# Kernel tuning notes

Hardware: AMD Instinct MI355X
Metric: run time of the kernel (lower is better)

## Reference

```python
import jax, jax.numpy as jnp
import numpy as np

B, C, P, NP = 16, 768, 2048, 64
FFE = 4


def _ln(x, g, b, eps=1e-5):
    m = jnp.mean(x, axis=-1, keepdims=True)
    v = jnp.mean(jnp.square(x - m), axis=-1, keepdims=True)
    return (x - m) * jax.lax.rsqrt(v + eps) * g + b


def _gelu(x):
    return jax.nn.gelu(x, approximate=False)  # torch nn.GELU default (erf)


def _any_attn(q, k, v, nqg, nqb, nkg, nkb, nvg, nvb, wq, wk, wv, wp, bq, bk, bv, bp):
    # AnyAttention: LN each stream, project, ReLU-gated logits scaled by d^-0.5, softmax, proj
    scale = q.shape[-1] ** -0.5
    qn = _ln(q, nqg, nqb) @ wq + bq
    kn = _ln(k, nkg, nkb) @ wk + bk
    vn = _ln(v, nvg, nvb) @ wv + bv
    attn = jnp.einsum('bqc,bkc->bqk', qn, kn)
    attn = jax.nn.relu(attn) * scale  # returned attn is relu*scale (pre-softmax)
    out = jnp.einsum('bqk,bkc->bqc', jax.nn.softmax(attn, axis=-1), vn)
    return attn, out @ wp + bp


def _forward(x, parts,
             enc_nq_g, enc_nq_b, enc_nk_g, enc_nk_b, enc_nv_g, enc_nv_b,
             enc_wq, enc_wk, enc_wv, enc_wp, enc_bq, enc_bk, enc_bv, enc_bp,
             dec_nq_g, dec_nq_b, dec_nk_g, dec_nk_b, dec_nv_g, dec_nv_b,
             dec_wq, dec_wk, dec_wv, dec_wp, dec_bq, dec_bk, dec_bv, dec_bp,
             ffn_ng, ffn_nb, ffn_w1, ffn_b1, ffn_w2, ffn_b2,
             sr_w1, sr_b1, sr_w2, sr_b2):
    x = jnp.swapaxes(x, 1, 2)  # b c p -> b p c
    # SimpleReasoning: SE-style gate over part tokens (AdaptiveMaxPool1d(1) = max over channel dim)
    g = jnp.max(parts, axis=-1)                                  # [b, np]
    g = _gelu(g @ sr_w1 + sr_b1)
    gate = jax.nn.sigmoid(g @ sr_w2 + sr_b2)[..., None]          # [b, np, 1]
    parts = gate * parts + parts                                 # parts1 + parts (residual)
    # enc_attn: parts attend over image tokens
    attn0, attn_out = _any_attn(parts, x, x,
                                enc_nq_g, enc_nq_b, enc_nk_g, enc_nk_b, enc_nv_g, enc_nv_b,
                                enc_wq, enc_wk, enc_wv, enc_wp, enc_bq, enc_bk, enc_bv, enc_bp)
    attn_0 = jnp.max(attn0, axis=-1)                             # maxpool over k -> [b, np]
    parts_in = parts + attn_out
    # FFN on image tokens with residual
    h = _ln(x, ffn_ng, ffn_nb)
    feats1 = x + (_gelu(h @ ffn_w1 + ffn_b1) @ ffn_w2 + ffn_b2)
    # dec_attn: image tokens attend over part tokens
    _, feats = _any_attn(feats1, parts_in, parts_in,
                         dec_nq_g, dec_nq_b, dec_nk_g, dec_nk_b, dec_nv_g, dec_nv_b,
                         dec_wq, dec_wk, dec_wv, dec_wp, dec_bq, dec_bk, dec_bv, dec_bp)
    feats = x + feats
    return jnp.swapaxes(feats, 1, 2), attn_0                     # [b, c, p], [b, np]


def setup_inputs() -> dict:
    key = jax.random.key(0)
    ki = iter(jax.random.split(key, 48))
    def rn(shape, s=1.0):
        return jax.random.normal(next(ki), shape, jnp.float32) * s
    d = {}
    d['x'] = rn((B, C, P))
    d['parts'] = rn((B, NP, C))
    for pre in ('enc', 'dec'):
        for nm in ('nq', 'nk', 'nv'):
            d[f'{pre}_{nm}_g'] = jnp.ones((C,), jnp.float32)
            d[f'{pre}_{nm}_b'] = jnp.zeros((C,), jnp.float32)
        for nm in ('wq', 'wk', 'wv', 'wp'):
            d[f'{pre}_{nm}'] = rn((C, C), 0.02)
        for nm in ('bq', 'bk', 'bv', 'bp'):
            d[f'{pre}_{nm}'] = jnp.zeros((C,), jnp.float32)
    d['ffn_ng'] = jnp.ones((C,), jnp.float32)
    d['ffn_nb'] = jnp.zeros((C,), jnp.float32)
    d['ffn_w1'] = rn((C, FFE * C), 0.02)
    d['ffn_b1'] = jnp.zeros((FFE * C,), jnp.float32)
    d['ffn_w2'] = rn((FFE * C, C), 0.02)
    d['ffn_b2'] = jnp.zeros((C,), jnp.float32)
    d['sr_w1'] = rn((NP, NP), 0.1)
    d['sr_b1'] = jnp.zeros((NP,), jnp.float32)
    d['sr_w2'] = rn((NP, NP), 0.1)
    d['sr_b2'] = jnp.zeros((NP,), jnp.float32)
    return d


def reference(x, parts,
              enc_nq_g, enc_nq_b, enc_nk_g, enc_nk_b, enc_nv_g, enc_nv_b,
              enc_wq, enc_wk, enc_wv, enc_wp, enc_bq, enc_bk, enc_bv, enc_bp,
              dec_nq_g, dec_nq_b, dec_nk_g, dec_nk_b, dec_nv_g, dec_nv_b,
              dec_wq, dec_wk, dec_wv, dec_wp, dec_bq, dec_bk, dec_bv, dec_bp,
              ffn_ng, ffn_nb, ffn_w1, ffn_b1, ffn_w2, ffn_b2,
              sr_w1, sr_b1, sr_w2, sr_b2):
    return _forward(x, parts,
                    enc_nq_g, enc_nq_b, enc_nk_g, enc_nk_b, enc_nv_g, enc_nv_b,
                    enc_wq, enc_wk, enc_wv, enc_wp, enc_bq, enc_bk, enc_bv, enc_bp,
                    dec_nq_g, dec_nq_b, dec_nk_g, dec_nk_b, dec_nv_g, dec_nv_b,
                    dec_wq, dec_wk, dec_wv, dec_wp, dec_bq, dec_bk, dec_bv, dec_bp,
                    ffn_ng, ffn_nb, ffn_w1, ffn_b1, ffn_w2, ffn_b2,
                    sr_w1, sr_b1, sr_w2, sr_b2)
```

## Files before the change

kernel.cpp:

```cpp
#include <hip/hip_runtime.h>

typedef unsigned short u16;
typedef unsigned int u32;
typedef __bf16 bf16x8 __attribute__((ext_vector_type(8)));
typedef float f32x4 __attribute__((ext_vector_type(4)));
typedef unsigned int u32x4 __attribute__((ext_vector_type(4)));

#define BB 16
#define CC 768
#define PP 2048
#define FF 3072

__device__ __forceinline__ float b2f(u16 u) {
  unsigned int x = ((unsigned int)u) << 16;
  return __builtin_bit_cast(float, x);
}
__device__ __forceinline__ u16 f2b(float f) {
  unsigned int x = __builtin_bit_cast(unsigned int, f);
  x += 0x7fffu + ((x >> 16) & 1u);
  return (u16)(x >> 16);
}
__device__ __forceinline__ float erf_fast(float x) {
  float ax = fabsf(x);
  float t = 1.0f / fmaf(0.3275911f, ax, 1.0f);
  float p = t * fmaf(t, fmaf(t, fmaf(t, fmaf(t, 1.061405429f, -1.453152027f),
                                     1.421413741f), -0.284496736f), 0.254829592f);
  float r = 1.0f - p * __expf(-ax * ax);
  return copysignf(r, x);
}
__device__ __forceinline__ float gelu_f(float x) {
  return 0.5f * x * (1.0f + erf_fast(x * 0.7071067811865475f));
}

typedef __attribute__((address_space(1))) const unsigned int g_u32;
typedef __attribute__((address_space(3))) unsigned int l_u32;
__device__ __forceinline__ void gl_lds16(const u16* g, u16* l) {
  __builtin_amdgcn_global_load_lds((g_u32*)g, (l_u32*)l, 16, 0, 0);
}

struct Wtr10 {
  const float* W[10]; const float* g[10]; u16* O[10]; int Kd[10]; int Nd[10];
};
__global__ void wtr10_k(Wtr10 a) {
  __shared__ float t[64][65];
  int tbid = blockIdx.x;
  int z, bx, by;
  if (tbid < 1152) { z = tbid / 144; int r = tbid % 144; bx = r % 12; by = r / 12; }
  else if (tbid < 1728) { z = 8; int r = tbid - 1152; bx = r % 48; by = r / 48; }
  else { z = 9; int r = tbid - 1728; bx = r % 12; by = r / 12; }
  const float* W = a.W[z];
  const float* g = a.g[z];
  u16* Wt = a.O[z];
  int K = a.Kd[z], N = a.Nd[z];
  int n0 = bx * 64, k0 = by * 64;
  int tx = threadIdx.x & 63, ty = threadIdx.x >> 6;
  for (int i = 0; i < 16; ++i) {
    int k = k0 + ty + i * 4;
    float sc = g ? g[k] : 1.0f;
    t[ty + i * 4][tx] = W[(long)k * N + n0 + tx] * sc;
  }
  __syncthreads();
  for (int i = 0; i < 16; ++i) {
    int n = n0 + ty + i * 4;
    Wt[(long)n * K + k0 + tx] = f2b(t[tx][ty + i * 4]);
  }
}

struct Bf7 {
  const float* b[7]; const float* nb[7]; const float* W[7]; float* o[7];
  int Kd[7]; int Nd[7];
};
__global__ void bfuse7_k(Bf7 a) {
  __shared__ float red[4][64];
  int tbid = blockIdx.x;
  int z, bx;
  if (tbid < 72) { z = tbid / 12; bx = tbid % 12; }
  else { z = 6; bx = tbid - 72; }
  const float* b = a.b[z];
  const float* nb = a.nb[z];
  const float* W = a.W[z];
  float* outb = a.o[z];
  int K = a.Kd[z], N = a.Nd[z];
  int n = bx * 64 + (threadIdx.x & 63);
  int slice = threadIdx.x >> 6;
  float acc = 0.f;
#pragma unroll 4
  for (int k = slice; k < K; k += 4) acc += nb[k] * W[(long)k * N + n];
  red[slice][threadIdx.x & 63] = acc;
  __syncthreads();
  if (slice == 0)
    outb[n] = b[n] + red[0][threadIdx.x & 63] + red[1][threadIdx.x & 63] +
              red[2][threadIdx.x & 63] + red[3][threadIdx.x & 63];
}

__global__ void xprep_k(const float* __restrict__ x, float* __restrict__ mean,
                        float* __restrict__ rstd, u16* __restrict__ xh) {
  __shared__ float t[64][65];
  __shared__ float red[8][64];
  __shared__ float mn_s[64], rs_s[64];
  int p0 = blockIdx.x * 64, b = blockIdx.y;
  int tx = threadIdx.x & 63, ty = threadIdx.x >> 6;
  const float* xb = x + (long)b * CC * PP;
  float s = 0.f, sq = 0.f;
  for (int c = ty; c < CC; c += 4) {
    float f = xb[(long)c * PP + p0 + tx];
    s += f; sq += f * f;
  }
  red[ty][tx] = s;
  red[4 + ty][tx] = sq;
  __syncthreads();
  if (ty == 0) {
    float S = red[0][tx] + red[1][tx] + red[2][tx] + red[3][tx];
    float Q = red[4][tx] + red[5][tx] + red[6][tx] + red[7][tx];
    float m = S * (1.0f / 768.0f);
    float var = Q * (1.0f / 768.0f) - m * m;
    float rs = rsqrtf(var + 1e-5f);
    mn_s[tx] = m; rs_s[tx] = rs;
    int gi = (b << 11) + p0 + tx;
    mean[gi] = m; rstd[gi] = rs;
  }
  __syncthreads();
  u16* ob = xh + (long)b * PP * CC;
  for (int cb = 0; cb < 12; ++cb) {
    int c0 = cb * 64;
    for (int i = 0; i < 16; ++i)
      t[ty + i * 4][tx] = xb[(long)(c0 + ty + i * 4) * PP + p0 + tx];
    __syncthreads();
    for (int i = 0; i < 16; ++i) {
      int pl = ty + i * 4;
      ob[(long)(p0 + pl) * CC + c0 + tx] = f2b((t[tx][pl] - mn_s[pl]) * rs_s[pl]);
    }
    __syncthreads();
  }
}

__global__ void parts_gate_k(const float* __restrict__ parts,
                             const float* __restrict__ w1, const float* __restrict__ b1,
                             const float* __restrict__ w2, const float* __restrict__ b2,
                             float* __restrict__ gate_out) {
  int b = blockIdx.x, t = threadIdx.x;
  __shared__ float g[64], g1[64];
  int r = t >> 2, l4 = t & 3;
  const float* pr = parts + ((long)b * 64 + r) * CC;
  float m = -1e30f;
  for (int c = l4; c < CC; c += 4) m = fmaxf(m, pr[c]);
  m = fmaxf(m, __shfl_xor(m, 1));
  m = fmaxf(m, __shfl_xor(m, 2));
  if (l4 == 0) g[r] = m;
  __syncthreads();
  if (t < 64) {
    float a = b1[t];
    for (int k = 0; k < 64; ++k) a += g[k] * w1[k * 64 + t];
    g1[t] = gelu_f(a);
  }
  __syncthreads();
  if (t < 64) {
    float a = b2[t];
    for (int k = 0; k < 64; ++k) a += g1[k] * w2[k * 64 + t];
    gate_out[b * 64 + t] = 1.0f / (1.0f + expf(-a));
  }
}

__global__ void gate_ln_k(const float* __restrict__ parts, const float* __restrict__ gate,
                          float* __restrict__ parts1, u16* __restrict__ ph) {
  int row = blockIdx.x * 4 + (threadIdx.x >> 6);
  int lane = threadIdx.x & 63;
  float g = 1.0f + gate[row];
  const float* ip = parts + (long)row * CC;
  float* op1 = parts1 + (long)row * CC;
  float v[12];
  float s = 0.f, sq = 0.f;
  for (int i = 0; i < 12; ++i) {
    float f = ip[lane + i * 64] * g;
    v[i] = f; op1[lane + i * 64] = f;
    s += f; sq += f * f;
  }
  for (int o = 32; o; o >>= 1) { s += __shfl_xor(s, o); sq += __shfl_xor(sq, o); }
  float mean = s * (1.0f / 768.0f);
  float var = sq * (1.0f / 768.0f) - mean * mean;
  float rstd = rsqrtf(var + 1e-5f);
  u16* op = ph + (long)row * CC;
  for (int i = 0; i < 12; ++i) op[lane + i * 64] = f2b((v[i] - mean) * rstd);
}

template <typename T>
__global__ void ln_rows_k(const T* __restrict__ in, u16* __restrict__ outp, int rows) {
  int row = blockIdx.x * 4 + (threadIdx.x >> 6);
  if (row >= rows) return;
  int lane = threadIdx.x & 63;
  const T* ip = in + (long)row * CC;
  float v[12];
  float s = 0.f, sq = 0.f;
  for (int i = 0; i < 12; ++i) {
    float f;
    if constexpr (sizeof(T) == 2) f = b2f(((const u16*)ip)[lane + i * 64]);
    else f = ((const float*)ip)[lane + i * 64];
    v[i] = f; s += f; sq += f * f;
  }
  for (int o = 32; o; o >>= 1) { s += __shfl_xor(s, o); sq += __shfl_xor(sq, o); }
  float mean = s * (1.0f / 768.0f);
  float var = sq * (1.0f / 768.0f) - mean * mean;
  float rstd = rsqrtf(var + 1e-5f);
  u16* op = outp + (long)row * CC;
  for (int i = 0; i < 12; ++i) op[lane + i * 64] = f2b((v[i] - mean) * rstd);
}

__global__ void softmax_enc_k(const float* __restrict__ attn, u16* __restrict__ sm,
                              float* __restrict__ attn0) {
  int row = blockIdx.x * 4 + (threadIdx.x >> 6);
  int lane = threadIdx.x & 63;
  const float* ap = attn + (long)row * PP;
  float v[32];
  float m = -1e30f;
  for (int i = 0; i < 32; ++i) { v[i] = ap[lane + i * 64]; m = fmaxf(m, v[i]); }
  for (int o = 32; o; o >>= 1) m = fmaxf(m, __shfl_xor(m, o));
  float s = 0.f;
  for (int i = 0; i < 32; ++i) { float e = expf(v[i] - m); v[i] = e; s += e; }
  for (int o = 32; o; o >>= 1) s += __shfl_xor(s, o);
  float inv = 1.0f / s;
  u16* sp = sm + (long)row * PP;
  for (int i = 0; i < 32; ++i) sp[lane + i * 64] = f2b(v[i] * inv);
  if (lane == 0) attn0[row] = m;
}

__global__ void pvred_k(const float* __restrict__ part, u16* __restrict__ outp) {
  long i = (long)blockIdx.x * 256 + threadIdx.x;
  const f32x4* p = (const f32x4*)part;
  f32x4 a = p[i];
  a += p[i + 196608];
  a += p[i + 2 * 196608];
  a += p[i + 3 * 196608];
  u32 lo = (u32)f2b(a.x) | ((u32)f2b(a.y) << 16);
  u32 hi = (u32)f2b(a.z) | ((u32)f2b(a.w) << 16);
  ((u32*)outp)[i * 2] = lo;
  ((u32*)outp)[i * 2 + 1] = hi;
}

template <int EPI>
__global__ __launch_bounds__(256) void gemmf_k(
    const u16* __restrict__ A, const u16* __restrict__ Bm, void* __restrict__ Cm,
    const float* __restrict__ bias, int M, int N, int K,
    const u16* __restrict__ rxh, const float* __restrict__ rmean,
    const float* __restrict__ rrstd, long rro, const float* __restrict__ res32) {
  __shared__ __align__(16) u16 As[128 * 32];
  __shared__ __align__(16) u16 Bs[128 * 32];
  const int nbx = N >> 7;
  const int nwg = gridDim.x;
  int tile = blockIdx.x;
  if ((nwg & 7) == 0) {
    tile = (tile & 7) * (nwg >> 3) + (tile >> 3);
  }
  const int bm0 = (tile / nbx) << 7;
  const int bn0 = (tile % nbx) << 7;
  const int tid = threadIdx.x;
  const int lane = tid & 63;
  const int wave = tid >> 6;
  const int laneq = lane & 15, lanek = lane >> 4;
  const int wm = (wave >> 1) << 6, wn = (wave & 1) << 6;
  const int srow = wave * 32 + (lane >> 2);
  const int scol = (lane & 3) << 3;
  const u16* Ag0 = A + (long)(bm0 + srow) * K + scol;
  const u16* Ag1 = A + (long)(bm0 + srow + 16) * K + scol;
  const u16* Bg0 = Bm + (long)(bn0 + srow) * K + scol;
  const u16* Bg1 = Bm + (long)(bn0 + srow + 16) * K + scol;
  u16* lA0 = As + wave * 1024;
  u16* lA1 = As + wave * 1024 + 512;
  u16* lB0 = Bs + wave * 1024;
  u16* lB1 = Bs + wave * 1024 + 512;
  f32x4 acc[4][4] = {};
  for (int k0 = 0; k0 < K; k0 += 32) {
    gl_lds16(Ag0 + k0, lA0);
    gl_lds16(Ag1 + k0, lA1);
    gl_lds16(Bg0 + k0, lB0);
    gl_lds16(Bg1 + k0, lB1);
    __syncthreads();
    bf16x8 af[4], bfr[4];
#pragma unroll
    for (int i = 0; i < 4; ++i)
      af[i] = *(const bf16x8*)(As + (wm + i * 16 + laneq) * 32 + (lanek << 3));
#pragma unroll
    for (int i = 0; i < 4; ++i)
      bfr[i] = *(const bf16x8*)(Bs + (wn + i * 16 + laneq) * 32 + (lanek << 3));
#pragma unroll
    for (int mi = 0; mi < 4; ++mi)
#pragma unroll
      for (int ni = 0; ni < 4; ++ni)
        acc[mi][ni] =
            __builtin_amdgcn_mfma_f32_16x16x32_bf16(af[mi], bfr[ni], acc[mi][ni], 0, 0, 0);
    __syncthreads();
  }
#pragma unroll
  for (int mi = 0; mi < 4; ++mi) {
#pragma unroll
    for (int r = 0; r < 4; ++r) {
      const int row = bm0 + wm + mi * 16 + (lanek << 2) + r;
      float mn = 0.f, istd = 0.f;
      if constexpr (EPI == 3) {
        long gr = rro + row;
        mn = rmean[gr];
        istd = 1.0f / rrstd[gr];
      }
#pragma unroll
      for (int ni = 0; ni < 4; ++ni) {
        const int col = bn0 + wn + ni * 16 + laneq;
        float v = acc[mi][ni][r] + bias[col];
        long off = (long)row * N + col;
        if constexpr (EPI == 0) {
          ((u16*)Cm)[off] = f2b(v);
        } else if constexpr (EPI == 1) {
          ((u16*)Cm)[off] = f2b(gelu_f(v));
        } else if constexpr (EPI == 3) {
          v += b2f(rxh[(rro + row) * 768 + col]) * istd + mn;
          ((u16*)Cm)[off] = f2b(v);
        } else {
          ((float*)Cm)[off] = v + res32[off];
        }
      }
    }
  }
}

#define G256_BAR() __builtin_amdgcn_s_barrier()
#define G256_WLGKM0()                                    \
  do {                                                   \
    asm volatile("s_waitcnt lgkmcnt(0)" ::: "memory");   \
    __builtin_amdgcn_sched_barrier(0);                   \
  } while (0)
#define G256_RD_A(HALF)                                                        \
  _Pragma("unroll") for (int m2 = 0; m2 < 4; ++m2) {                           \
    af[m2 * 2 + 0] = *(const bf16x8*)(Ab + ar + (HALF)*4096 + m2 * 1024 + g0); \
    af[m2 * 2 + 1] = *(const bf16x8*)(Ab + ar + (HALF)*4096 + m2 * 1024 + g1); \
  }
#define G256_RD_B(HALF, BFR)                                                   \
  _Pragma("unroll") for (int n2 = 0; n2 < 2; ++n2) {                           \
    BFR[n2 * 2 + 0] = *(const bf16x8*)(Bb + br + (HALF)*2048 + n2 * 1024 + g0);\
    BFR[n2 * 2 + 1] = *(const bf16x8*)(Bb + br + (HALF)*2048 + n2 * 1024 + g1);\
  }
#define G256_MFMA_Q(H, NH, BFR)                                                \
  __builtin_amdgcn_s_setprio(1);                                               \
  _Pragma("unroll") for (int m2 = 0; m2 < 4; ++m2)                             \
  _Pragma("unroll") for (int n2 = 0; n2 < 2; ++n2)                             \
  _Pragma("unroll") for (int s = 0; s < 2; ++s)                                \
      acc[(H)*4 + m2][(NH)*2 + n2] = __builtin_amdgcn_mfma_f32_16x16x32_bf16(  \
          af[m2 * 2 + s], BFR[n2 * 2 + s], acc[(H)*4 + m2][(NH)*2 + n2], 0, 0, 0); \
  __builtin_amdgcn_s_setprio(0);

template <int EPI>
__global__ __launch_bounds__(512, 2) void gemm256_k(
    const u16* __restrict__ A, const u16* __restrict__ Bm, void* __restrict__ Cm,
    const float* __restrict__ bias, int M, int N, int K,
    const u16* __restrict__ rxh, const float* __restrict__ rmean,
    const float* __restrict__ rrstd, long rro) {
  __shared__ __align__(16) u16 As[2 * 16384];
  __shared__ __align__(16) u16 Bs[2 * 16384];
  const int nbx = N >> 8;
  const int nwg = gridDim.x;
  int tile = blockIdx.x;
  if ((nwg & 7) == 0) {
    tile = (tile & 7) * (nwg >> 3) + (tile >> 3);
  }
  const int bm0 = (tile / nbx) << 8;
  const int bn0 = (tile % nbx) << 8;
  const int tid = threadIdx.x;
  const int lane = tid & 63;
  const int wave = tid >> 6;
  const int laneq = lane & 15, lanek = lane >> 4;
  const int wrow = (wave >> 2) << 7;
  const int wcol = (wave & 3) << 6;
  const int srow8 = lane >> 3;
  const int sg = (lane & 7) ^ srow8;
  const u16* gA = A + (long)(bm0 + wave * 8 + srow8) * K + sg * 8;
  const u16* gB = Bm + (long)(bn0 + wave * 8 + srow8) * K + sg * 8;
  const long lineK = (long)64 * K;
  const int ldsLine = wave * 512;
  const int gx = laneq & 7;
  const int g0 = ((lanek) ^ gx) << 3;
  const int g1 = ((lanek + 4) ^ gx) << 3;
  const int ar = (wrow + laneq) * 64;
  const int br = (wcol + laneq) * 64;
  f32x4 acc[8][4] = {};
  bf16x8 af[8], bfr0[4], bfr1[4];
  const int NT = K >> 6;

  {
    u16* dA = (u16*)As;
    u16* dB = (u16*)Bs;
    gl_lds16(gA, dA + ldsLine);
    gl_lds16(gA + lineK, dA + ldsLine + 4096);
    gl_lds16(gA + 2 * lineK, dA + ldsLine + 8192);
    gl_lds16(gA + 3 * lineK, dA + ldsLine + 12288);
    gl_lds16(gB, dB + ldsLine);
    gl_lds16(gB + lineK, dB + ldsLine + 4096);
    gl_lds16(gB + 2 * lineK, dB + ldsLine + 8192);
    gl_lds16(gB + 3 * lineK, dB + ldsLine + 12288);
  }
  for (int T = 0; T < NT; ++T) {
    const u16* Ab = As + (T & 1) * 16384;
    const u16* Bb = Bs + (T & 1) * 16384;
    u16* An = (u16*)As + ((T & 1) ^ 1) * 16384;
    u16* Bn = (u16*)Bs + ((T & 1) ^ 1) * 16384;
    const long ko = (long)(T + 1) * 64;
    const bool more = (T + 1 < NT);
    if (more) {
      gl_lds16(gA + ko, An + ldsLine);
      gl_lds16(gA + ko + lineK, An + ldsLine + 4096);
      gl_lds16(gB + ko, Bn + ldsLine);
      gl_lds16(gB + ko + lineK, Bn + ldsLine + 4096);
      asm volatile("s_waitcnt vmcnt(4)" ::: "memory");
    } else {
      asm volatile("s_waitcnt vmcnt(0)" ::: "memory");
    }
    G256_BAR();
    G256_RD_A(0);
    G256_RD_B(0, bfr0);
    G256_WLGKM0();
    G256_MFMA_Q(0, 0, bfr0);
    G256_BAR();
    if (more) {
      gl_lds16(gA + ko + 2 * lineK, An + ldsLine + 8192);
      gl_lds16(gA + ko + 3 * lineK, An + ldsLine + 12288);
      gl_lds16(gB + ko + 2 * lineK, Bn + ldsLine + 8192);
      gl_lds16(gB + ko + 3 * lineK, Bn + ldsLine + 12288);
    }
    G256_RD_B(1, bfr1);
    G256_BAR();
    G256_WLGKM0();
    G256_MFMA_Q(0, 1, bfr1);
    G256_BAR();
    G256_RD_A(1);
    G256_BAR();
    G256_WLGKM0();
    G256_MFMA_Q(1, 1, bfr1);
    G256_BAR();
    G256_MFMA_Q(1, 0, bfr0);
  }

#pragma unroll
  for (int mi = 0; mi < 8; ++mi) {
#pragma unroll
    for (int r = 0; r < 4; ++r) {
      const int row = bm0 + wrow + mi * 16 + (lanek << 2) + r;
      float mn = 0.f, istd = 0.f;
      if constexpr (EPI == 3) {
        long gr = rro + row;
        mn = rmean[gr];
        istd = 1.0f / rrstd[gr];
      }
#pragma unroll
      for (int ni = 0; ni < 4; ++ni) {
        const int col = bn0 + wcol + ni * 16 + laneq;
        float v = acc[mi][ni][r] + bias[col];
        long off = (long)row * N + col;
        if constexpr (EPI == 0) {
          ((u16*)Cm)[off] = f2b(v);
        } else if constexpr (EPI == 1) {
          ((u16*)Cm)[off] = f2b(gelu_f(v));
        } else {
          v += b2f(rxh[(rro + row) * 768 + col]) * istd + mn;
          ((u16*)Cm)[off] = f2b(v);
        }
      }
    }
  }
}

template <int EPI, bool BNT, int TM, int TN>
__global__ __launch_bounds__(256) void gemm_k(
    const u16* __restrict__ A, const u16* __restrict__ Bm, void* __restrict__ Cm,
    const float* __restrict__ bias, int M, int N, int kLen, int lda, int ldB,
    long sA, long sB, long sC, float scale, const float* __restrict__ res32) {
  __shared__ __align__(16) u16 As[TM][40];
  __shared__ __align__(16) u16 Bs[TN][40];
  const int bn0 = blockIdx.x * TN;
  const int bm0 = (EPI == 4) ? 0 : blockIdx.y * TM;
  const int kOff = (EPI == 4) ? blockIdx.y * kLen : 0;
  const int bz = blockIdx.z;
  const u16* Ab = A + (long)bz * sA;
  const u16* Bb = Bm + (long)bz * sB;
  const long coff = (EPI == 4) ? ((long)blockIdx.y * gridDim.z + bz) * sC
                               : (long)bz * sC;
  const int tid = threadIdx.x;
  const int lane = tid & 63;
  const int wave = tid >> 6;
  const int wm = (TM == 64) ? 0 : ((TN == 64) ? wave * 32 : ((wave >> 1) << 6));
  const int wn = (TN == 64) ? 0 : ((TM == 64) ? wave * 32 : ((wave & 1) << 6));
  constexpr int MI = (TN == 64) ? 2 : 4;
  constexpr int NI = (TM == 64) ? 2 : 4;
  const int laneq = lane & 15, lanek = lane >> 4;
  f32x4 acc[MI][NI] = {};
  for (int k0 = 0; k0 < kLen; k0 += 32) {
    __syncthreads();
#pragma unroll
    for (int j = 0; j < TM / 64; ++j) {
      int v = tid + j * 256;
      int m = v >> 2, kcl = (v & 3) << 3;
      u32x4 val = {0, 0, 0, 0};
      if (bm0 + m < M)
        val = *(const u32x4*)(Ab + (long)(bm0 + m) * lda + kOff + k0 + kcl);
      *(u32x4*)(&As[m][kcl]) = val;
    }
    if constexpr (BNT) {
#pragma unroll
      for (int j = 0; j < TN / 64; ++j) {
        int v = tid + j * 256;
        int n = v >> 2, kcl = (v & 3) << 3;
        u32x4 val = {0, 0, 0, 0};
        if (bn0 + n < N)
          val = *(const u32x4*)(Bb + (long)(bn0 + n) * ldB + kOff + k0 + kcl);
        *(u32x4*)(&Bs[n][kcl]) = val;
      }
    } else {
      constexpr int CCH = TN / 8;
#pragma unroll
      for (int j = 0; j < TN / 64; ++j) {
        int v = tid + j * 256;
        int kk = v / CCH, nc = (v % CCH) << 3;
        u32x4 val = {0, 0, 0, 0};
        if (bn0 + nc < N)
          val = *(const u32x4*)(Bb + (long)(kOff + k0 + kk) * ldB + bn0 + nc);
        union { u32x4 v4; u16 u[8]; } uu;
        uu.v4 = val;
#pragma unroll
        for (int e = 0; e < 8; ++e) Bs[nc + e][kk] = uu.u[e];
      }
    }
    __syncthreads();
    bf16x8 af[MI], bfr[NI];
#pragma unroll
    for (int i = 0; i < MI; ++i)
      af[i] = *(const bf16x8*)(&As[wm + i * 16 + laneq][lanek << 3]);
#pragma unroll
    for (int i = 0; i < NI; ++i)
      bfr[i] = *(const bf16x8*)(&Bs[wn + i * 16 + laneq][lanek << 3]);
#pragma unroll
    for (int mi = 0; mi < MI; ++mi)
#pragma unroll
      for (int ni = 0; ni < NI; ++ni)
        acc[mi][ni] =
            __builtin_amdgcn_mfma_f32_16x16x32_bf16(af[mi], bfr[ni], acc[mi][ni], 0, 0, 0);
  }
  if constexpr (EPI == 5) {
    __syncthreads();
    float* smem = (float*)(wave < 2 ? (void*)As : (void*)Bs) + (wave & 1) * 1024;
    const int pbase = bm0 + wm + (lane & 3) * 16;
    const long obase = (long)bz * CC * PP;
#pragma unroll
    for (int ni = 0; ni < 4; ++ni) {
#pragma unroll
      for (int mi = 0; mi < 4; ++mi)
#pragma unroll
        for (int r = 0; r < 4; ++r) {
          const int col = bn0 + wn + ni * 16 + laneq;
          smem[(mi * 16 + (lanek << 2) + r) * 16 + laneq] = acc[mi][ni][r] + bias[col];
        }
      const int c = bn0 + wn + ni * 16 + (lane >> 2);
      const float* xs = res32 + obase + (long)c * PP + pbase;
      float* os = (float*)Cm + obase + (long)c * PP + pbase;
      const float* sr = smem + (lane & 3) * 256 + (lane >> 2);
#pragma unroll
      for (int q4 = 0; q4 < 4; ++q4) {
        f32x4 xv = *(const f32x4*)(xs + q4 * 4);
        f32x4 ov;
        ov.x = sr[(q4 * 4 + 0) * 16] + xv.x;
        ov.y = sr[(q4 * 4 + 1) * 16] + xv.y;
        ov.z = sr[(q4 * 4 + 2) * 16] + xv.z;
        ov.w = sr[(q4 * 4 + 3) * 16] + xv.w;
        *(f32x4*)(os + q4 * 4) = ov;
      }
    }
  } else if constexpr (EPI == 6) {
#pragma unroll
    for (int mi = 0; mi < MI; ++mi) {
#pragma unroll
      for (int r = 0; r < 4; ++r) {
        float e[NI];
        float mx = -1e30f;
#pragma unroll
        for (int ni = 0; ni < NI; ++ni) {
          float v = fmaxf(acc[mi][ni][r], 0.0f) * scale;
          e[ni] = v;
          mx = fmaxf(mx, v);
        }
        mx = fmaxf(mx, __shfl_xor(mx, 1));
        mx = fmaxf(mx, __shfl_xor(mx, 2));
        mx = fmaxf(mx, __shfl_xor(mx, 4));
        mx = fmaxf(mx, __shfl_xor(mx, 8));
        float s = 0.f;
#pragma unroll
        for (int ni = 0; ni < NI; ++ni) { e[ni] = __expf(e[ni] - mx); s += e[ni]; }
        s += __shfl_xor(s, 1);
        s += __shfl_xor(s, 2);
        s += __shfl_xor(s, 4);
        s += __shfl_xor(s, 8);
        float inv = 1.0f / s;
        const int row = bm0 + wm + mi * 16 + (lanek << 2) + r;
#pragma unroll
        for (int ni = 0; ni < NI; ++ni) {
          const int col = bn0 + wn + ni * 16 + laneq;
          ((u16*)Cm)[coff + (long)row * N + col] = f2b(e[ni] * inv);
        }
      }
    }
  } else {
#pragma unroll
    for (int mi = 0; mi < MI; ++mi) {
#pragma unroll
      for (int ni = 0; ni < NI; ++ni) {
        int col = bn0 + wn + ni * 16 + laneq;
        if (col >= N) continue;
#pragma unroll
        for (int r = 0; r < 4; ++r) {
          int row = bm0 + wm + mi * 16 + (lanek << 2) + r;
          if (row >= M) continue;
          float v = acc[mi][ni][r];
          long off = coff + (long)row * N + col;
          if constexpr (EPI == 0) {
            if (bias) v += bias[col];
            ((u16*)Cm)[off] = f2b(v);
          } else if constexpr (EPI == 2) {
            ((float*)Cm)[off] = fmaxf(v, 0.0f) * scale;
          } else {
            ((float*)Cm)[off] = v;
          }
        }
      }
    }
  }
}

extern "C" void kernel_launch(void* const* d_in, const int* in_sizes, int n_in,
                              void* d_out, int out_size, void* d_ws, size_t ws_size,
                              hipStream_t stream) {
  (void)in_sizes; (void)n_in; (void)out_size;
  const float* x        = (const float*)d_in[0];
  const float* parts    = (const float*)d_in[1];
  const float* enc_nq_g = (const float*)d_in[2];
  const float* enc_nq_b = (const float*)d_in[3];
  const float* enc_nk_g = (const float*)d_in[4];
  const float* enc_nk_b = (const float*)d_in[5];
  const float* enc_nv_g = (const float*)d_in[6];
  const float* enc_nv_b = (const float*)d_in[7];
  const float* enc_wq   = (const float*)d_in[8];
  const float* enc_wk   = (const float*)d_in[9];
  const float* enc_wv   = (const float*)d_in[10];
  const float* enc_wp   = (const float*)d_in[11];
  const float* enc_bq   = (const float*)d_in[12];
  const float* enc_bk   = (const float*)d_in[13];
  const float* enc_bv   = (const float*)d_in[14];
  const float* enc_bp   = (const float*)d_in[15];
  const float* dec_nq_g = (const float*)d_in[16];
  const float* dec_nq_b = (const float*)d_in[17];
  const float* dec_nk_g = (const float*)d_in[18];
  const float* dec_nk_b = (const float*)d_in[19];
  const float* dec_nv_g = (const float*)d_in[20];
  const float* dec_nv_b = (const float*)d_in[21];
  const float* dec_wq   = (const float*)d_in[22];
  const float* dec_wk   = (const float*)d_in[23];
  const float* dec_wv   = (const float*)d_in[24];
  const float* dec_wp   = (const float*)d_in[25];
  const float* dec_bq   = (const float*)d_in[26];
  const float* dec_bk   = (const float*)d_in[27];
  const float* dec_bv   = (const float*)d_in[28];
  const float* dec_bp   = (const float*)d_in[29];
  const float* ffn_ng   = (const float*)d_in[30];
  const float* ffn_nb   = (const float*)d_in[31];
  const float* ffn_w1   = (const float*)d_in[32];
  const float* ffn_b1   = (const float*)d_in[33];
  const float* ffn_w2   = (const float*)d_in[34];
  const float* ffn_b2   = (const float*)d_in[35];
  const float* sr_w1    = (const float*)d_in[36];
  const float* sr_b1    = (const float*)d_in[37];
  const float* sr_w2    = (const float*)d_in[38];
  const float* sr_b2    = (const float*)d_in[39];
  float* outp = (float*)d_out;

  char* base = (char*)d_ws;
  size_t used = 0;
  auto alloc = [&](size_t bytes) -> void* {
    void* p = base + used;
    used += (bytes + 255) & ~(size_t)255;
    return p;
  };
  const long MC = (long)CC * CC;
  u16* WqeT  = (u16*)alloc(MC * 2);
  u16* WkvT  = (u16*)alloc(MC * 2 * 2);
  u16* WpeT  = (u16*)alloc(MC * 2);
  u16* WqdT  = (u16*)alloc(MC * 2);
  u16* WkvdT = (u16*)alloc(MC * 2 * 2);
  u16* WpdT  = (u16*)alloc(MC * 2);
  u16* W1T   = (u16*)alloc((long)CC * FF * 2);
  u16* W2T   = (u16*)alloc((long)CC * FF * 2);
  float* bqe  = (float*)alloc(CC * 4);
  float* bkv  = (float*)alloc(2 * CC * 4);
  float* bqd  = (float*)alloc(CC * 4);
  float* bkvd = (float*)alloc(2 * CC * 4);
  float* b1f  = (float*)alloc(FF * 4);
  float* meanx = (float*)alloc((long)BB * PP * 4);
  float* rstdx = (float*)alloc((long)BB * PP * 4);
  const long BPC = (long)BB * PP * CC;
  u16* bufA = (u16*)alloc(BPC * 2);
  u16* bufB = (u16*)alloc(BPC * 2);
  u16* bufC = (u16*)alloc(BPC * 2);
  u16* kv = bufB;
  const long PC = (long)BB * 64 * CC;
  float* parts1   = (float*)alloc(PC * 4);
  float* gateb    = (float*)alloc((long)BB * 64 * 4);
  u16*   p1hat    = (u16*)alloc(PC * 2);
  u16*   qn_e     = (u16*)alloc(PC * 2);
  float* attn_e   = (float*)alloc((long)BB * 64 * PP * 4);
  u16*   sm_e     = (u16*)alloc((long)BB * 64 * PP * 2);
  u16*   pv_e     = (u16*)alloc(PC * 2);
  float* pvpart   = (float*)alloc((long)4 * PC * 4);
  float* parts_in = (float*)alloc(PC * 4);
  u16*   pin_hat  = (u16*)alloc(PC * 2);
  u16*   kvd      = (u16*)alloc(PC * 2 * 2);
  u16*   vwT      = (u16*)alloc(PC * 2);
  u16*   sm_d     = (u16*)alloc((long)BB * PP * 64 * 2);
  int chunk_rows = 16384;
  while (chunk_rows > 4096 &&
         used + (size_t)chunk_rows * FF * 2 > ws_size)
    chunk_rows >>= 1;
  u16* ff1 = (u16*)alloc((long)chunk_rows * FF * 2);
  if (used > ws_size) return;

  const float scale = 0.03608439182435161f;
  dim3 blk(256);
  dim3 blk2(512);

  {
    Wtr10 wa;
    const float* Ws[10] = {enc_wq, enc_wk, enc_wv, enc_wp, dec_wq, dec_wk,
                           dec_wv, dec_wp, ffn_w1, ffn_w2};
    const float* gs[10] = {enc_nq_g, enc_nk_g, enc_nv_g, nullptr, dec_nq_g,
                           dec_nk_g, dec_nv_g, nullptr, ffn_ng, nullptr};
    u16* Os[10] = {WqeT, WkvT, WkvT + MC, WpeT, WqdT, WkvdT, WkvdT + MC, WpdT,
                   W1T, W2T};
    int Ks[10] = {CC, CC, CC, CC, CC, CC, CC, CC, CC, FF};
    int Ns[10] = {CC, CC, CC, CC, CC, CC, CC, CC, FF, CC};
    for (int i = 0; i < 10; ++i) {
      wa.W[i] = Ws[i]; wa.g[i] = gs[i]; wa.O[i] = Os[i];
      wa.Kd[i] = Ks[i]; wa.Nd[i] = Ns[i];
    }
    wtr10_k<<<2304, blk, 0, stream>>>(wa);
    Bf7 ba;
    const float* bs[7] = {enc_bq, enc_bk, enc_bv, dec_bq, dec_bk, dec_bv, ffn_b1};
    const float* nbs[7] = {enc_nq_b, enc_nk_b, enc_nv_b, dec_nq_b, dec_nk_b,
                           dec_nv_b, ffn_nb};
    const float* ws[7] = {enc_wq, enc_wk, enc_wv, dec_wq, dec_wk, dec_wv, ffn_w1};
    float* os[7] = {bqe, bkv, bkv + CC, bqd, bkvd, bkvd + CC, b1f};
    int Ks2[7] = {CC, CC, CC, CC, CC, CC, CC};
    int Ns2[7] = {CC, CC, CC, CC, CC, CC, FF};
    for (int i = 0; i < 7; ++i) {
      ba.b[i] = bs[i]; ba.nb[i] = nbs[i]; ba.W[i] = ws[i]; ba.o[i] = os[i];
      ba.Kd[i] = Ks2[i]; ba.Nd[i] = Ns2[i];
    }
    bfuse7_k<<<120, blk, 0, stream>>>(ba);
  }

  xprep_k<<<dim3(32, 16), blk, 0, stream>>>(x, meanx, rstdx, bufA);

  parts_gate_k<<<16, blk, 0, stream>>>(parts, sr_w1, sr_b1, sr_w2, sr_b2, gateb);
  gate_ln_k<<<256, blk, 0, stream>>>(parts, gateb, parts1, p1hat);

  gemmf_k<0><<<48, blk, 0, stream>>>(p1hat, WqeT, qn_e, bqe, 1024, CC, CC,
      nullptr, nullptr, nullptr, 0, nullptr);
  gemm256_k<0><<<768, blk2, 0, stream>>>(bufA, WkvT, kv, bkv, 32768, 2 * CC, CC,
      nullptr, nullptr, nullptr, 0);

  gemm_k<2, true, 64, 128><<<dim3(16, 1, 16), blk, 0, stream>>>(
      qn_e, kv, attn_e, nullptr, 64, PP, CC, CC, 2 * CC,
      (long)64 * CC, (long)PP * 2 * CC, (long)64 * PP, scale, nullptr);
  softmax_enc_k<<<256, blk, 0, stream>>>(attn_e, sm_e, outp + (long)BB * CC * PP);
  gemm_k<4, false, 64, 128><<<dim3(6, 4, 16), blk, 0, stream>>>(
      sm_e, kv + CC, pvpart, nullptr, 64, CC, PP / 4, PP, 2 * CC,
      (long)64 * PP, (long)PP * 2 * CC, (long)64 * CC, 0.f, nullptr);
  pvred_k<<<768, blk, 0, stream>>>(pvpart, pv_e);
  gemmf_k<4><<<48, blk, 0, stream>>>(pv_e, WpeT, parts_in, enc_bp, 1024, CC, CC,
      nullptr, nullptr, nullptr, 0, parts1);

  ln_rows_k<float><<<256, blk, 0, stream>>>(parts_in, pin_hat, 1024);
  gemmf_k<0><<<96, blk, 0, stream>>>(pin_hat, WkvdT, kvd, bkvd, 1024, 2 * CC, CC,
      nullptr, nullptr, nullptr, 0, nullptr);
  gemm_k<0, true, 128, 64><<<dim3(1, 6, 16), blk, 0, stream>>>(
      WpdT, kvd + CC, vwT, nullptr, CC, 64, CC, CC, 2 * CC,
      0, (long)64 * 2 * CC, (long)CC * 64, 0.f, nullptr);

  for (long r0 = 0; r0 < 32768; r0 += chunk_rows) {
    gemm256_k<1><<<(chunk_rows / 256) * 12, blk2, 0, stream>>>(
        bufA + r0 * CC, W1T, ff1, b1f, chunk_rows, FF, CC,
        nullptr, nullptr, nullptr, 0);
    gemm256_k<3><<<(chunk_rows / 256) * 3, blk2, 0, stream>>>(
        ff1, W2T, bufB + r0 * CC, ffn_b2, chunk_rows, CC, FF,
        bufA, meanx, rstdx, r0);
  }
  ln_rows_k<u16><<<8192, blk, 0, stream>>>(bufB, bufB, 32768);
  gemmf_k<0><<<1536, blk, 0, stream>>>(bufB, WqdT, bufC, bqd, 32768, CC, CC,
      nullptr, nullptr, nullptr, 0, nullptr);

  gemm_k<6, true, 128, 64><<<dim3(1, 16, 16), blk, 0, stream>>>(
      bufC, kvd, sm_d, nullptr, PP, 64, CC, CC, 2 * CC,
      (long)PP * CC, (long)64 * 2 * CC, (long)PP * 64, scale, nullptr);

  gemm_k<5, true, 128, 128><<<dim3(6, 16, 16), blk, 0, stream>>>(
      sm_d, vwT, outp, dec_bp, PP, CC, 64, 64, 64,
      (long)PP * 64, (long)CC * 64, 0, 0.f, x);
}
```

Baseline: 1.179 ms.

## Reassociate attention projections to skip K/V and decoder-Q projections on image tokens

Encoder logits are computed as (qn·Wk^T)·x̂ plus a q·bk row term, so the large K projection over all 32768 image tokens is no longer needed. Attention-weighted values use x̂ directly, with Wv·Wp folded into one matrix and a matching bias. The decoder query projection over image tokens is folded into the small key side (kvd·Wq^T plus a bias dot). This removes two big GEMMs over the token dimension in exchange for a few small GEMMs, dot kernels and changed summation order, which affects bf16 rounding.

After: 1.107 ms. 1.07x faster.

```diff
diff --git a/kernel.cpp b/kernel.cpp
--- a/kernel.cpp
+++ b/kernel.cpp
@@ -39,21 +39,30 @@
 }
 
 struct Wtr10 {
-  const float* W[10]; const float* g[10]; u16* O[10]; int Kd[10]; int Nd[10];
+  const float* W[10]; const float* g[10]; u16* O[10];
+  int Kd[10]; int Nd[10]; int tr[10]; int cum[11];
 };
 __global__ void wtr10_k(Wtr10 a) {
   __shared__ float t[64][65];
   int tbid = blockIdx.x;
-  int z, bx, by;
-  if (tbid < 1152) { z = tbid / 144; int r = tbid % 144; bx = r % 12; by = r / 12; }
-  else if (tbid < 1728) { z = 8; int r = tbid - 1152; bx = r % 48; by = r / 48; }
-  else { z = 9; int r = tbid - 1728; bx = r % 12; by = r / 12; }
+  int z = 0;
+  while (tbid >= a.cum[z + 1]) ++z;
+  int r = tbid - a.cum[z];
   const float* W = a.W[z];
   const float* g = a.g[z];
   u16* Wt = a.O[z];
   int K = a.Kd[z], N = a.Nd[z];
-  int n0 = bx * 64, k0 = by * 64;
+  int nbx = N >> 6;
+  int n0 = (r % nbx) * 64, k0 = (r / nbx) * 64;
   int tx = threadIdx.x & 63, ty = threadIdx.x >> 6;
+  if (!a.tr[z]) {
+    for (int i = 0; i < 16; ++i) {
+      int k = k0 + ty + i * 4;
+      float sc = g ? g[k] : 1.0f;
+      Wt[(long)k * N + n0 + tx] = f2b(W[(long)k * N + n0 + tx] * sc);
+    }
+    return;
+  }
   for (int i = 0; i < 16; ++i) {
     int k = k0 + ty + i * 4;
     float sc = g ? g[k] : 1.0f;
@@ -93,6 +102,32 @@
               red[2][threadIdx.x & 63] + red[3][threadIdx.x & 63];
 }
 
+__global__ void bfuse1_k(const float* __restrict__ b, const float* __restrict__ nb,
+                         const float* __restrict__ W, float* __restrict__ outb) {
+  __shared__ float red[4][64];
+  int n = blockIdx.x * 64 + (threadIdx.x & 63);
+  int slice = threadIdx.x >> 6;
+  float acc = 0.f;
+#pragma unroll 4
+  for (int k = slice; k < CC; k += 4) acc += nb[k] * W[(long)k * CC + n];
+  red[slice][threadIdx.x & 63] = acc;
+  __syncthreads();
+  if (slice == 0)
+    outb[n] = b[n] + red[0][threadIdx.x & 63] + red[1][threadIdx.x & 63] +
+              red[2][threadIdx.x & 63] + red[3][threadIdx.x & 63];
+}
+
+__global__ void dot_k(const u16* __restrict__ A, int stride,
+                      const float* __restrict__ vec, float* __restrict__ outp) {
+  int row = blockIdx.x * 4 + (threadIdx.x >> 6);
+  int lane = threadIdx.x & 63;
+  const u16* ip = A + (long)row * stride;
+  float s = 0.f;
+  for (int i = 0; i < 12; ++i) s += b2f(ip[lane + i * 64]) * vec[lane + i * 64];
+  for (int o = 32; o; o >>= 1) s += __shfl_xor(s, o);
+  if (lane == 0) outp[row] = s;
+}
+
 __global__ void xprep_k(const float* __restrict__ x, float* __restrict__ mean,
                         float* __restrict__ rstd, u16* __restrict__ xh) {
   __shared__ float t[64][65];
@@ -239,9 +274,8 @@
 template <int EPI>
 __global__ __launch_bounds__(256) void gemmf_k(
     const u16* __restrict__ A, const u16* __restrict__ Bm, void* __restrict__ Cm,
-    const float* __restrict__ bias, int M, int N, int K,
-    const u16* __restrict__ rxh, const float* __restrict__ rmean,
-    const float* __restrict__ rrstd, long rro, const float* __restrict__ res32) {
+    const float* __restrict__ bias, int M, int N, int K, int lda,
+    const float* __restrict__ res32) {
   __shared__ __align__(16) u16 As[128 * 32];
   __shared__ __align__(16) u16 Bs[128 * 32];
   const int nbx = N >> 7;
@@ -259,8 +293,8 @@
   const int wm = (wave >> 1) << 6, wn = (wave & 1) << 6;
   const int srow = wave * 32 + (lane >> 2);
   const int scol = (lane & 3) << 3;
-  const u16* Ag0 = A + (long)(bm0 + srow) * K + scol;
-  const u16* Ag1 = A + (long)(bm0 + srow + 16) * K + scol;
+  const u16* Ag0 = A + (long)(bm0 + srow) * lda + scol;
+  const u16* Ag1 = A + (long)(bm0 + srow + 16) * lda + scol;
   const u16* Bg0 = Bm + (long)(bn0 + srow) * K + scol;
   const u16* Bg1 = Bm + (long)(bn0 + srow + 16) * K + scol;
   u16* lA0 = As + wave * 1024;
@@ -294,23 +328,12 @@
 #pragma unroll
     for (int r = 0; r < 4; ++r) {
       const int row = bm0 + wm + mi * 16 + (lanek << 2) + r;
-      float mn = 0.f, istd = 0.f;
-      if constexpr (EPI == 3) {
-        long gr = rro + row;
-        mn = rmean[gr];
-        istd = 1.0f / rrstd[gr];
-      }
 #pragma unroll
       for (int ni = 0; ni < 4; ++ni) {
         const int col = bn0 + wn + ni * 16 + laneq;
-        float v = acc[mi][ni][r] + bias[col];
+        float v = acc[mi][ni][r] + (bias ? bias[col] : 0.f);
         long off = (long)row * N + col;
         if constexpr (EPI == 0) {
-          ((u16*)Cm)[off] = f2b(v);
-        } else if constexpr (EPI == 1) {
-          ((u16*)Cm)[off] = f2b(gelu_f(v));
-        } else if constexpr (EPI == 3) {
-          v += b2f(rxh[(rro + row) * 768 + col]) * istd + mn;
           ((u16*)Cm)[off] = f2b(v);
         } else {
           ((float*)Cm)[off] = v + res32[off];
@@ -468,7 +491,8 @@
 __global__ __launch_bounds__(256) void gemm_k(
     const u16* __restrict__ A, const u16* __restrict__ Bm, void* __restrict__ Cm,
     const float* __restrict__ bias, int M, int N, int kLen, int lda, int ldB,
-    long sA, long sB, long sC, float scale, const float* __restrict__ res32) {
+    long sA, long sB, long sC, float scale, const float* __restrict__ res32,
+    const float* __restrict__ radd) {
   __shared__ __align__(16) u16 As[TM][40];
   __shared__ __align__(16) u16 Bs[TN][40];
   const int bn0 = blockIdx.x * TN;
@@ -577,7 +601,9 @@
         float mx = -1e30f;
 #pragma unroll
         for (int ni = 0; ni < NI; ++ni) {
-          float v = fmaxf(acc[mi][ni][r], 0.0f) * scale;
+          const int col = bn0 + wn + ni * 16 + laneq;
+          float v = acc[mi][ni][r] + (radd ? radd[(long)bz * N + col] : 0.f);
+          v = fmaxf(v, 0.0f) * scale;
           e[ni] = v;
           mx = fmaxf(mx, v);
         }
@@ -618,6 +644,7 @@
             if (bias) v += bias[col];
             ((u16*)Cm)[off] = f2b(v);
           } else if constexpr (EPI == 2) {
+            v += radd ? radd[(long)bz * M + row] : 0.f;
             ((float*)Cm)[off] = fmaxf(v, 0.0f) * scale;
           } else {
             ((float*)Cm)[off] = v;
@@ -683,37 +710,42 @@
   };
   const long MC = (long)CC * CC;
   u16* WqeT  = (u16*)alloc(MC * 2);
-  u16* WkvT  = (u16*)alloc(MC * 2 * 2);
   u16* WpeT  = (u16*)alloc(MC * 2);
-  u16* WqdT  = (u16*)alloc(MC * 2);
   u16* WkvdT = (u16*)alloc(MC * 2 * 2);
   u16* WpdT  = (u16*)alloc(MC * 2);
   u16* W1T   = (u16*)alloc((long)CC * FF * 2);
   u16* W2T   = (u16*)alloc((long)CC * FF * 2);
+  u16* WkS   = (u16*)alloc(MC * 2);
+  u16* WvS   = (u16*)alloc(MC * 2);
+  u16* WqdS  = (u16*)alloc(MC * 2);
   float* bqe  = (float*)alloc(CC * 4);
   float* bkv  = (float*)alloc(2 * CC * 4);
   float* bqd  = (float*)alloc(CC * 4);
   float* bkvd = (float*)alloc(2 * CC * 4);
   float* b1f  = (float*)alloc(FF * 4);
+  float* bias2 = (float*)alloc(CC * 4);
   float* meanx = (float*)alloc((long)BB * PP * 4);
   float* rstdx = (float*)alloc((long)BB * PP * 4);
   const long BPC = (long)BB * PP * CC;
   u16* bufA = (u16*)alloc(BPC * 2);
   u16* bufB = (u16*)alloc(BPC * 2);
-  u16* bufC = (u16*)alloc(BPC * 2);
-  u16* kv = bufB;
   const long PC = (long)BB * 64 * CC;
   float* parts1   = (float*)alloc(PC * 4);
   float* gateb    = (float*)alloc((long)BB * 64 * 4);
   u16*   p1hat    = (u16*)alloc(PC * 2);
   u16*   qn_e     = (u16*)alloc(PC * 2);
+  u16*   qtil     = (u16*)alloc(PC * 2);
+  float* qdotv    = (float*)alloc((long)BB * 64 * 4);
   float* attn_e   = (float*)alloc((long)BB * 64 * PP * 4);
   u16*   sm_e     = (u16*)alloc((long)BB * 64 * PP * 2);
   u16*   pv_e     = (u16*)alloc(PC * 2);
   float* pvpart   = (float*)alloc((long)4 * PC * 4);
+  u16*   m2w      = (u16*)alloc(MC * 2);
   float* parts_in = (float*)alloc(PC * 4);
   u16*   pin_hat  = (u16*)alloc(PC * 2);
   u16*   kvd      = (u16*)alloc(PC * 2 * 2);
+  u16*   gmat     = (u16*)alloc(PC * 2);
+  float* kdotv    = (float*)alloc((long)BB * 64 * 4);
   u16*   vwT      = (u16*)alloc(PC * 2);
   u16*   sm_d     = (u16*)alloc((long)BB * PP * 64 * 2);
   int chunk_rows = 16384;
@@ -729,19 +761,24 @@
 
   {
     Wtr10 wa;
-    const float* Ws[10] = {enc_wq, enc_wk, enc_wv, enc_wp, dec_wq, dec_wk,
-                           dec_wv, dec_wp, ffn_w1, ffn_w2};
-    const float* gs[10] = {enc_nq_g, enc_nk_g, enc_nv_g, nullptr, dec_nq_g,
-                           dec_nk_g, dec_nv_g, nullptr, ffn_ng, nullptr};
-    u16* Os[10] = {WqeT, WkvT, WkvT + MC, WpeT, WqdT, WkvdT, WkvdT + MC, WpdT,
-                   W1T, W2T};
-    int Ks[10] = {CC, CC, CC, CC, CC, CC, CC, CC, CC, FF};
-    int Ns[10] = {CC, CC, CC, CC, CC, CC, CC, CC, FF, CC};
+    const float* Ws[10] = {enc_wq, dec_wk, dec_wv, enc_wp, dec_wp,
+                           ffn_w1, ffn_w2, enc_wk, enc_wv, dec_wq};
+    const float* gs[10] = {enc_nq_g, dec_nk_g, dec_nv_g, nullptr, nullptr,
+                           ffn_ng, nullptr, enc_nk_g, enc_nv_g, dec_nq_g};
+    u16* Os[10] = {WqeT, WkvdT, WkvdT + MC, WpeT, WpdT, W1T, W2T, WkS, WvS, WqdS};
+    int Ks[10] = {CC, CC, CC, CC, CC, CC, FF, CC, CC, CC};
+    int Ns[10] = {CC, CC, CC, CC, CC, FF, CC, CC, CC, CC};
+    int tr[10] = {1, 1, 1, 1, 1, 1, 1, 0, 0, 0};
+    int blks[10];
+    int cum = 0;
     for (int i = 0; i < 10; ++i) {
+      blks[i] = (Ns[i] / 64) * (Ks[i] / 64);
       wa.W[i] = Ws[i]; wa.g[i] = gs[i]; wa.O[i] = Os[i];
-      wa.Kd[i] = Ks[i]; wa.Nd[i] = Ns[i];
-    }
-    wtr10_k<<<2304, blk, 0, stream>>>(wa);
+      wa.Kd[i] = Ks[i]; wa.Nd[i] = Ns[i]; wa.tr[i] = tr[i];
+      wa.cum[i] = cum; cum += blks[i];
+    }
+    wa.cum[10] = cum;
+    wtr10_k<<<cum, blk, 0, stream>>>(wa);
     Bf7 ba;
     const float* bs[7] = {enc_bq, enc_bk, enc_bv, dec_bq, dec_bk, dec_bv, ffn_b1};
     const float* nbs[7] = {enc_nq_b, enc_nk_b, enc_nv_b, dec_nq_b, dec_nk_b,
@@ -755,35 +792,43 @@
       ba.Kd[i] = Ks2[i]; ba.Nd[i] = Ns2[i];
     }
     bfuse7_k<<<120, blk, 0, stream>>>(ba);
-  }
+    bfuse1_k<<<12, blk, 0, stream>>>(enc_bp, bkv + CC, enc_wp, bias2);
+  }
+
+  gemmf_k<0><<<36, blk, 0, stream>>>(WpeT, WvS, m2w, nullptr, CC, CC, CC, CC,
+      nullptr);
 
   xprep_k<<<dim3(32, 16), blk, 0, stream>>>(x, meanx, rstdx, bufA);
 
   parts_gate_k<<<16, blk, 0, stream>>>(parts, sr_w1, sr_b1, sr_w2, sr_b2, gateb);
   gate_ln_k<<<256, blk, 0, stream>>>(parts, gateb, parts1, p1hat);
 
-  gemmf_k<0><<<48, blk, 0, stream>>>(p1hat, WqeT, qn_e, bqe, 1024, CC, CC,
-      nullptr, nullptr, nullptr, 0, nullptr);
-  gemm256_k<0><<<768, blk2, 0, stream>>>(bufA, WkvT, kv, bkv, 32768, 2 * CC, CC,
-      nullptr, nullptr, nullptr, 0);
+  gemmf_k<0><<<48, blk, 0, stream>>>(p1hat, WqeT, qn_e, bqe, 1024, CC, CC, CC,
+      nullptr);
+  gemmf_k<0><<<48, blk, 0, stream>>>(qn_e, WkS, qtil, nullptr, 1024, CC, CC, CC,
+      nullptr);
+  dot_k<<<256, blk, 0, stream>>>(qn_e, CC, bkv, qdotv);
 
   gemm_k<2, true, 64, 128><<<dim3(16, 1, 16), blk, 0, stream>>>(
-      qn_e, kv, attn_e, nullptr, 64, PP, CC, CC, 2 * CC,
-      (long)64 * CC, (long)PP * 2 * CC, (long)64 * PP, scale, nullptr);
+      qtil, bufA, attn_e, nullptr, 64, PP, CC, CC, CC,
+      (long)64 * CC, (long)PP * CC, (long)64 * PP, scale, nullptr, qdotv);
   softmax_enc_k<<<256, blk, 0, stream>>>(attn_e, sm_e, outp + (long)BB * CC * PP);
   gemm_k<4, false, 64, 128><<<dim3(6, 4, 16), blk, 0, stream>>>(
-      sm_e, kv + CC, pvpart, nullptr, 64, CC, PP / 4, PP, 2 * CC,
-      (long)64 * PP, (long)PP * 2 * CC, (long)64 * CC, 0.f, nullptr);
+      sm_e, bufA, pvpart, nullptr, 64, CC, PP / 4, PP, CC,
+      (long)64 * PP, (long)PP * CC, (long)64 * CC, 0.f, nullptr, nullptr);
   pvred_k<<<768, blk, 0, stream>>>(pvpart, pv_e);
-  gemmf_k<4><<<48, blk, 0, stream>>>(pv_e, WpeT, parts_in, enc_bp, 1024, CC, CC,
-      nullptr, nullptr, nullptr, 0, parts1);
+  gemmf_k<4><<<48, blk, 0, stream>>>(pv_e, m2w, parts_in, bias2, 1024, CC, CC, CC,
+      parts1);
 
   ln_rows_k<float><<<256, blk, 0, stream>>>(parts_in, pin_hat, 1024);
   gemmf_k<0><<<96, blk, 0, stream>>>(pin_hat, WkvdT, kvd, bkvd, 1024, 2 * CC, CC,
-      nullptr, nullptr, nullptr, 0, nullptr);
+      CC, nullptr);
+  gemmf_k<0><<<48, blk, 0, stream>>>(kvd, WqdS, gmat, nullptr, 1024, CC, CC,
+      2 * CC, nullptr);
+  dot_k<<<256, blk, 0, stream>>>(kvd, 2 * CC, bqd, kdotv);
   gemm_k<0, true, 128, 64><<<dim3(1, 6, 16), blk, 0, stream>>>(
       WpdT, kvd + CC, vwT, nullptr, CC, 64, CC, CC, 2 * CC,
-      0, (long)64 * 2 * CC, (long)CC * 64, 0.f, nullptr);
+      0, (long)64 * 2 * CC, (long)CC * 64, 0.f, nullptr, nullptr);
 
   for (long r0 = 0; r0 < 32768; r0 += chunk_rows) {
     gemm256_k<1><<<(chunk_rows / 256) * 12, blk2, 0, stream>>>(
@@ -794,14 +839,12 @@
         bufA, meanx, rstdx, r0);
   }
   ln_rows_k<u16><<<8192, blk, 0, stream>>>(bufB, bufB, 32768);
-  gemmf_k<0><<<1536, blk, 0, stream>>>(bufB, WqdT, bufC, bqd, 32768, CC, CC,
-      nullptr, nullptr, nullptr, 0, nullptr);
 
   gemm_k<6, true, 128, 64><<<dim3(1, 16, 16), blk, 0, stream>>>(
-      bufC, kvd, sm_d, nullptr, PP, 64, CC, CC, 2 * CC,
-      (long)PP * CC, (long)64 * 2 * CC, (long)PP * 64, scale, nullptr);
+      bufB, gmat, sm_d, nullptr, PP, 64, CC, CC, CC,
+      (long)PP * CC, (long)64 * CC, (long)PP * 64, scale, nullptr, kdotv);
 
   gemm_k<5, true, 128, 128><<<dim3(6, 16, 16), blk, 0, stream>>>(
       sm_d, vwT, outp, dec_bp, PP, CC, 64, 64, 64,
-      (long)PP * 64, (long)CC * 64, 0, 0.f, x);
-}
+      (long)PP * 64, (long)CC * 64, 0, 0.f, x, nullptr);
+}
```
